# Kernel optimization log

Hardware: AMD Instinct MI355X
Metric: run time of the kernel (lower is better)

Reference implementation:

```python
import jax, jax.numpy as jnp
import numpy as np

C_IN = 128
C_INNER = 128


def setup_inputs() -> dict:
    key = jax.random.key(0)
    ks = jax.random.split(key, 9)
    b, c, h, w = 4, C_IN, 64, 64
    s = 1.0 / np.sqrt(c)
    x = jax.random.normal(ks[0], (b, c, h, w), dtype=jnp.float32)
    Wq = jax.random.normal(ks[1], (C_INNER, C_IN), dtype=jnp.float32) * s
    bq = jnp.zeros((C_INNER,), dtype=jnp.float32)
    Wk = jax.random.normal(ks[2], (C_INNER, C_IN), dtype=jnp.float32) * s
    bk = jnp.zeros((C_INNER,), dtype=jnp.float32)
    Wv = jax.random.normal(ks[3], (C_INNER, C_IN), dtype=jnp.float32) * s
    bv = jnp.zeros((C_INNER,), dtype=jnp.float32)
    Wo = jax.random.normal(ks[4], (C_IN, C_INNER), dtype=jnp.float32) * (1.0 / np.sqrt(C_INNER))
    bo = jnp.zeros((C_IN,), dtype=jnp.float32)
    return {"x": x, "Wq": Wq, "bq": bq, "Wk": Wk, "bk": bk,
            "Wv": Wv, "bv": bv, "Wo": Wo, "bo": bo}


def _conv1x1(x, W, bias):
    # x: (b,c,h,w), W: (o,c) -> (b,o,h,w)
    return jnp.einsum('oc,bchw->bohw', W, x) + bias[None, :, None, None]


def reference(x, Wq, bq, Wk, bk, Wv, bv, Wo, bo):
    b, c, h, w = x.shape
    ci = Wq.shape[0]
    n = h * w
    q = _conv1x1(x, Wq, bq).reshape(b, ci, n)          # (b, ci, n)
    k = _conv1x1(x, Wk, bk).reshape(b, ci, n)          # (b, ci, n)
    v = _conv1x1(x, Wv, bv).reshape(b, ci, n)          # (b, ci, n)
    # attn = softmax(q^T @ k) over keys
    attn = jnp.einsum('bci,bcj->bij', q, k)            # (b, n, n)
    attn = jax.nn.softmax(attn, axis=-1)
    out = jnp.einsum('bij,bcj->bci', attn, v)          # (b, ci, n)
    out = out.reshape(b, ci, h, w)
    out = _conv1x1(out, Wo, bo)
    return out + x
```

## Files before the change

kernel.cpp:

```cpp
#include <hip/hip_runtime.h>
#include <math.h>
#include <stdint.h>

#define CDIM 128
#define NTOT 4096

typedef _Float16 f16x8 __attribute__((ext_vector_type(8)));
typedef float floatx4 __attribute__((ext_vector_type(4)));

static __device__ __forceinline__ floatx4 mfma16(f16x8 a, f16x8 b, floatx4 c) {
    return __builtin_amdgcn_mfma_f32_16x16x32_f16(a, b, c, 0, 0, 0);
}
static __device__ __forceinline__ unsigned short f2h(float f) {
    _Float16 h = (_Float16)f;
    return __builtin_bit_cast(unsigned short, h);
}
static __device__ __forceinline__ float h2f(unsigned short u) {
    return (float)__builtin_bit_cast(_Float16, u);
}

#define SWZ(row, cc) ((((row) << 7)) + ((((cc) ^ ((row) & 15))) << 3))
#define SWZ8(row, cc) ((((row) << 6)) + ((((cc) ^ ((row) & 7))) << 3))

static __device__ __forceinline__ void gload_lds16(const void* g, void* l) {
    __builtin_amdgcn_global_load_lds(
        (const __attribute__((address_space(1))) void*)g,
        (__attribute__((address_space(3))) void*)l, 16, 0, 0);
}

__global__ __launch_bounds__(256) void wcvt_kernel(
    const float* __restrict__ Wq, const float* __restrict__ Wk,
    const float* __restrict__ Wv, const float* __restrict__ Wo,
    unsigned short* __restrict__ Wh)
{
    const float* src = (blockIdx.y == 0) ? Wq : (blockIdx.y == 1) ? Wk
                     : (blockIdx.y == 2) ? Wv : Wo;
    const int i = (blockIdx.x * 256 + threadIdx.x) * 4;
    float4 f = *(const float4*)&src[i];
    ushort4 u = { f2h(f.x), f2h(f.y), f2h(f.z), f2h(f.w) };
    *(ushort4*)&Wh[(size_t)blockIdx.y * 16384 + i] = u;
}

__global__ __launch_bounds__(256) void qkv_proj_kernel(
    const float* __restrict__ x, const unsigned short* __restrict__ Wh,
    const float* __restrict__ bq, const float* __restrict__ bk,
    const float* __restrict__ bv,
    unsigned short* __restrict__ qo, unsigned short* __restrict__ ko,
    unsigned short* __restrict__ vo)
{
    __shared__ __align__(16) unsigned short Xs[64][136];

    const int t = threadIdx.x, b = blockIdx.y, n0 = blockIdx.x * 64;
    const int zo = blockIdx.z * 64;
    const int w = t >> 6, quad = (t >> 4) & 3, l15 = t & 15;

    {
        const int n = (t & 15) * 4;
        const int c = (t >> 4) * 8;
        float4 xr[8];
        #pragma unroll
        for (int j = 0; j < 8; ++j)
            xr[j] = *(const float4*)&x[((size_t)b * CDIM + c + j) * NTOT + n0 + n];
        #pragma unroll
        for (int k = 0; k < 4; ++k) {
            ushort4 ulo, uhi;
            ulo.x = f2h(((const float*)&xr[0])[k]);
            ulo.y = f2h(((const float*)&xr[1])[k]);
            ulo.z = f2h(((const float*)&xr[2])[k]);
            ulo.w = f2h(((const float*)&xr[3])[k]);
            uhi.x = f2h(((const float*)&xr[4])[k]);
            uhi.y = f2h(((const float*)&xr[5])[k]);
            uhi.z = f2h(((const float*)&xr[6])[k]);
            uhi.w = f2h(((const float*)&xr[7])[k]);
            *(ushort4*)&Xs[n + k][c]     = ulo;
            *(ushort4*)&Xs[n + k][c + 4] = uhi;
        }
    }
    __syncthreads();

    f16x8 xf[4];
    #pragma unroll
    for (int f = 0; f < 4; ++f)
        xf[f] = *(const f16x8*)&Xs[w * 16 + l15][f * 32 + quad * 8];

    #pragma unroll
    for (int s = 0; s < 2; ++s) {
        const unsigned short* Wm = Wh + (size_t)s * 16384;
        const float* bias = s ? bk : bq;
        unsigned short* dst = s ? ko : qo;
        #pragma unroll
        for (int ot = 0; ot < 4; ++ot) {
            floatx4 acc = (floatx4){0.f, 0.f, 0.f, 0.f};
            #pragma unroll
            for (int f = 0; f < 4; ++f) {
                f16x8 aW = *(const f16x8*)
                    &Wm[(size_t)(zo + ot * 16 + l15) * CDIM + f * 32 + quad * 8];
                acc = mfma16(aW, xf[f], acc);
            }
            const int ob = zo + ot * 16 + quad * 4;
            ushort4 u;
            u.x = f2h(acc[0] + bias[ob + 0]);
            u.y = f2h(acc[1] + bias[ob + 1]);
            u.z = f2h(acc[2] + bias[ob + 2]);
            u.w = f2h(acc[3] + bias[ob + 3]);
            *(ushort4*)&dst[((size_t)b * NTOT + n0 + w * 16 + l15) * CDIM + ob] = u;
        }
    }
    {
        const unsigned short* Wm = Wh + 2 * 16384;
        #pragma unroll
        for (int ot = 0; ot < 4; ++ot) {
            floatx4 acc = (floatx4){0.f, 0.f, 0.f, 0.f};
            #pragma unroll
            for (int f = 0; f < 4; ++f) {
                f16x8 bW = *(const f16x8*)
                    &Wm[(size_t)(zo + ot * 16 + l15) * CDIM + f * 32 + quad * 8];
                acc = mfma16(xf[f], bW, acc);
            }
            const int o = zo + ot * 16 + l15;
            const float bv_ = bv[o];
            ushort4 u;
            u.x = f2h(acc[0] + bv_); u.y = f2h(acc[1] + bv_);
            u.z = f2h(acc[2] + bv_); u.w = f2h(acc[3] + bv_);
            *(ushort4*)&vo[((size_t)b * CDIM + o) * NTOT + n0 + w * 16 + quad * 4] = u;
        }
    }
}

__global__ __launch_bounds__(256, 3) void attn_kernel(
    const unsigned short* __restrict__ qg,
    const unsigned short* __restrict__ kg,
    const unsigned short* __restrict__ vg,
    unsigned short* __restrict__ Op,
    float* __restrict__ Ms, float* __restrict__ Ls)
{
    __shared__ __align__(16) unsigned short Kb[2][64 * 128];
    __shared__ __align__(16) unsigned short Vs[128 * 64];

    const int t = threadIdx.x;
    const int w = t >> 6, quad = (t >> 4) & 3, l15 = t & 15;

    const int bid = blockIdx.x;
    const int swz = ((bid & 7) << 6) | (bid >> 3);
    const int gidx = swz >> 5;
    const int b = gidx & 3;
    const int z = gidx >> 2;
    const int i0 = (swz & 31) * 128;
    const int jbase = z * 1024;
    const size_t vbase = (size_t)b * CDIM * NTOT;

    f16x8 bQ[2][4];
    #pragma unroll
    for (int nt = 0; nt < 2; ++nt) {
        const size_t qrow = ((size_t)b * NTOT + i0 + w * 32 + nt * 16 + l15) * CDIM;
        #pragma unroll
        for (int f = 0; f < 4; ++f)
            bQ[nt][f] = *(const f16x8*)&qg[qrow + f * 32 + quad * 8];
    }

    auto stageK = [&](unsigned short* Kd, int j0) {
        const size_t kbase = ((size_t)b * NTOT + j0) * CDIM;
        #pragma unroll
        for (int r = 0; r < 4; ++r) {
            const int flat = r * 256 + t;
            const int ldsoff = (r * 256 + (t & ~63)) * 8;
            const int krow = flat >> 4, kcc = flat & 15;
            gload_lds16(&kg[kbase + (size_t)krow * CDIM + ((kcc ^ (krow & 15)) << 3)],
                        &Kd[ldsoff]);
        }
    };
    auto stageV = [&](int j0) {
        const size_t vrow0 = vbase + j0;
        #pragma unroll
        for (int r = 0; r < 4; ++r) {
            const int flat = r * 256 + t;
            const int ldsoff = (r * 256 + (t & ~63)) * 8;
            const int vrow = flat >> 3, vcc = flat & 7;
            gload_lds16(&vg[vrow0 + (size_t)vrow * NTOT + ((vcc ^ (vrow & 7)) << 3)],
                        &Vs[ldsoff]);
        }
    };

    floatx4 accO[2][8];
    #pragma unroll
    for (int nt = 0; nt < 2; ++nt)
        #pragma unroll
        for (int dt = 0; dt < 8; ++dt) accO[nt][dt] = (floatx4){0.f, 0.f, 0.f, 0.f};
    float m_run[2] = {-INFINITY, -INFINITY};
    float l_part[2] = {0.f, 0.f};

    stageK(Kb[0], jbase);

    for (int iter = 0; iter < 16; ++iter) {
        const int cur = iter & 1;
        const int j0 = jbase + iter * 64;

        asm volatile("s_waitcnt vmcnt(0) lgkmcnt(0)" ::: "memory");
        __builtin_amdgcn_s_barrier();

        stageV(j0);
        if (iter < 15) stageK(Kb[cur ^ 1], j0 + 64);

        floatx4 accT[2][4];
        #pragma unroll
        for (int nt = 0; nt < 2; ++nt)
            #pragma unroll
            for (int jt = 0; jt < 4; ++jt) accT[nt][jt] = (floatx4){0.f, 0.f, 0.f, 0.f};
        #pragma unroll
        for (int jt = 0; jt < 4; ++jt)
            #pragma unroll
            for (int f = 0; f < 4; ++f) {
                f16x8 aK = *(const f16x8*)&Kb[cur][SWZ(jt * 16 + l15, f * 4 + quad)];
                accT[0][jt] = mfma16(aK, bQ[0][f], accT[0][jt]);
                accT[1][jt] = mfma16(aK, bQ[1][f], accT[1][jt]);
            }

        ushort4 pu[2][4];
        #pragma unroll
        for (int nt = 0; nt < 2; ++nt) {
            float tm = accT[nt][0][0];
            #pragma unroll
            for (int jt = 0; jt < 4; ++jt)
                #pragma unroll
                for (int r = 0; r < 4; ++r) tm = fmaxf(tm, accT[nt][jt][r]);
            tm = fmaxf(tm, __shfl_xor(tm, 16));
            tm = fmaxf(tm, __shfl_xor(tm, 32));
            if (__ballot(tm > m_run[nt] + 8.f)) {
                const float m_new = fmaxf(m_run[nt], tm);
                const float alpha = __expf(m_run[nt] - m_new);
                m_run[nt] = m_new;
                l_part[nt] *= alpha;
                #pragma unroll
                for (int dt = 0; dt < 8; ++dt) {
                    accO[nt][dt][0] *= alpha; accO[nt][dt][1] *= alpha;
                    accO[nt][dt][2] *= alpha; accO[nt][dt][3] *= alpha;
                }
            }
            const float mcur = m_run[nt];
            float ps = 0.f;
            #pragma unroll
            for (int jt = 0; jt < 4; ++jt) {
                float p0 = __expf(accT[nt][jt][0] - mcur);
                float p1 = __expf(accT[nt][jt][1] - mcur);
                float p2 = __expf(accT[nt][jt][2] - mcur);
                float p3 = __expf(accT[nt][jt][3] - mcur);
                ps += (p0 + p1) + (p2 + p3);
                pu[nt][jt].x = f2h(p0); pu[nt][jt].y = f2h(p1);
                pu[nt][jt].z = f2h(p2); pu[nt][jt].w = f2h(p3);
            }
            l_part[nt] += ps;
        }

        if (iter < 15)
            asm volatile("s_waitcnt lgkmcnt(0) vmcnt(4)" ::: "memory");
        else
            asm volatile("s_waitcnt lgkmcnt(0) vmcnt(0)" ::: "memory");
        __builtin_amdgcn_s_barrier();

        unsigned short* Pb = Kb[cur];
        #pragma unroll
        for (int nt = 0; nt < 2; ++nt) {
            const int prow = w * 32 + nt * 16 + l15;
            #pragma unroll
            for (int jt = 0; jt < 4; ++jt)
                *(ushort4*)&Pb[SWZ8(prow, 2 * jt + (quad >> 1)) + (quad & 1) * 4] =
                    pu[nt][jt];
        }

        f16x8 bP[2][2];
        #pragma unroll
        for (int nt = 0; nt < 2; ++nt) {
            const int prow = w * 32 + nt * 16 + l15;
            #pragma unroll
            for (int kb = 0; kb < 2; ++kb)
                bP[nt][kb] = *(const f16x8*)&Pb[SWZ8(prow, kb * 4 + quad)];
        }
        #pragma unroll
        for (int dt = 0; dt < 8; ++dt)
            #pragma unroll
            for (int kb = 0; kb < 2; ++kb) {
                f16x8 aV = *(const f16x8*)&Vs[SWZ8(dt * 16 + l15, kb * 4 + quad)];
                accO[0][dt] = mfma16(aV, bP[0][kb], accO[0][dt]);
                accO[1][dt] = mfma16(aV, bP[1][kb], accO[1][dt]);
            }
    }

    #pragma unroll
    for (int nt = 0; nt < 2; ++nt) {
        float lf = l_part[nt];
        lf += __shfl_xor(lf, 16);
        lf += __shfl_xor(lf, 32);
        const float inv = 1.0f / lf;
        const size_t orow =
            (((size_t)z * 4 + b) * NTOT + i0 + w * 32 + nt * 16 + l15) * CDIM;
        #pragma unroll
        for (int dt = 0; dt < 8; ++dt) {
            ushort4 u;
            u.x = f2h(accO[nt][dt][0] * inv); u.y = f2h(accO[nt][dt][1] * inv);
            u.z = f2h(accO[nt][dt][2] * inv); u.w = f2h(accO[nt][dt][3] * inv);
            *(ushort4*)&Op[orow + dt * 16 + quad * 4] = u;
        }
        if (quad == 0) {
            const int idx = (z * 4 + b) * NTOT + i0 + w * 32 + nt * 16 + l15;
            Ms[idx] = m_run[nt];
            Ls[idx] = lf;
        }
    }
}

__global__ __launch_bounds__(256) void out_proj_kernel(
    const unsigned short* __restrict__ Op,
    const float* __restrict__ Ms, const float* __restrict__ Ls,
    const unsigned short* __restrict__ Woh, const float* __restrict__ bo,
    const float* __restrict__ x, float* __restrict__ out)
{
    __shared__ __align__(16) unsigned short As[64][136];

    const int t = threadIdx.x, b = blockIdx.y, n0 = blockIdx.x * 64;
    const int zo = blockIdx.z * 64;
    const int w = t >> 6, quad = (t >> 4) & 3, l15 = t & 15;

    const size_t PER = (size_t)NTOT * 4 * CDIM;

    #pragma unroll
    for (int r = 0; r < 4; ++r) {
        int flat = r * 256 + t;
        int row = flat >> 4, c16 = (flat & 15) * 8;
        const int bn = b * NTOT + n0 + row;
        float m0 = Ms[bn], m1 = Ms[bn + 16384], m2 = Ms[bn + 32768], m3 = Ms[bn + 49152];
        float M = fmaxf(fmaxf(m0, m1), fmaxf(m2, m3));
        float w0 = Ls[bn]         * __expf(m0 - M);
        float w1 = Ls[bn + 16384] * __expf(m1 - M);
        float w2 = Ls[bn + 32768] * __expf(m2 - M);
        float w3 = Ls[bn + 49152] * __expf(m3 - M);
        const float inv = 1.0f / (w0 + w1 + w2 + w3);
        w0 *= inv; w1 *= inv; w2 *= inv; w3 *= inv;

        const size_t base = (size_t)bn * CDIM + c16;
        uint4 a0 = *(const uint4*)&Op[base];
        uint4 a1 = *(const uint4*)&Op[PER + base];
        uint4 a2 = *(const uint4*)&Op[2 * PER + base];
        uint4 a3 = *(const uint4*)&Op[3 * PER + base];
        const unsigned short* p0 = (const unsigned short*)&a0;
        const unsigned short* p1 = (const unsigned short*)&a1;
        const unsigned short* p2 = (const unsigned short*)&a2;
        const unsigned short* p3 = (const unsigned short*)&a3;
        unsigned short mv[8];
        #pragma unroll
        for (int j = 0; j < 8; ++j)
            mv[j] = f2h(w0 * h2f(p0[j]) + w1 * h2f(p1[j]) +
                        w2 * h2f(p2[j]) + w3 * h2f(p3[j]));
        *(uint4*)&As[row][c16] = *(const uint4*)mv;
    }
    __syncthreads();

    f16x8 bA[4];
    #pragma unroll
    for (int f = 0; f < 4; ++f)
        bA[f] = *(const f16x8*)&As[w * 16 + l15][f * 32 + quad * 8];

    #pragma unroll
    for (int ot = 0; ot < 4; ++ot) {
        floatx4 acc = (floatx4){0.f, 0.f, 0.f, 0.f};
        #pragma unroll
        for (int f = 0; f < 4; ++f) {
            f16x8 aW = *(const f16x8*)
                &Woh[(size_t)(zo + ot * 16 + l15) * CDIM + f * 32 + quad * 8];
            acc = mfma16(aW, bA[f], acc);
        }
        const int ob = zo + ot * 16 + quad * 4;
        #pragma unroll
        for (int r = 0; r < 4; ++r) {
            size_t idx = ((size_t)b * CDIM + ob + r) * NTOT + n0 + w * 16 + l15;
            out[idx] = acc[r] + bo[ob + r] + x[idx];
        }
    }
}

extern "C" void kernel_launch(void* const* d_in, const int* in_sizes, int n_in,
                              void* d_out, int out_size, void* d_ws, size_t ws_size,
                              hipStream_t stream)
{
    const float* x  = (const float*)d_in[0];
    const float* Wq = (const float*)d_in[1];
    const float* bq = (const float*)d_in[2];
    const float* Wk = (const float*)d_in[3];
    const float* bk = (const float*)d_in[4];
    const float* Wv = (const float*)d_in[5];
    const float* bv = (const float*)d_in[6];
    const float* Wo = (const float*)d_in[7];
    const float* bo = (const float*)d_in[8];
    float* out = (float*)d_out;

    const size_t PER = (size_t)4 * CDIM * NTOT;
    unsigned short* q_ws  = (unsigned short*)d_ws;
    unsigned short* k_ws  = q_ws + PER;
    unsigned short* v_ws  = k_ws + PER;
    unsigned short* op_ws = v_ws + PER;
    float*          ms_ws = (float*)(op_ws + 4 * PER);
    float*          ls_ws = ms_ws + 4 * 16384;
    unsigned short* wh_ws = (unsigned short*)(ls_ws + 4 * 16384);

    wcvt_kernel<<<dim3(16, 4), dim3(256), 0, stream>>>(Wq, Wk, Wv, Wo, wh_ws);
    qkv_proj_kernel<<<dim3(64, 4, 2), dim3(256), 0, stream>>>(
        x, wh_ws, bq, bk, bv, q_ws, k_ws, v_ws);
    attn_kernel<<<dim3(512, 1, 1), dim3(256), 0, stream>>>(
        q_ws, k_ws, v_ws, op_ws, ms_ws, ls_ws);
    out_proj_kernel<<<dim3(64, 4, 2), dim3(256), 0, stream>>>(
        op_ws, ms_ws, ls_ws, wh_ws + 3 * 16384, bo, x, out);
}
```

Before: 161.4 us.

## Double-buffer V tiles in attention, add dedicated P buffer, retile projection kernels

Result: faster. 150.5 us (-6.7%).

```diff
diff --git a/kernel.cpp b/kernel.cpp
--- a/kernel.cpp
+++ b/kernel.cpp
@@ -48,32 +48,28 @@
     unsigned short* __restrict__ qo, unsigned short* __restrict__ ko,
     unsigned short* __restrict__ vo)
 {
-    __shared__ __align__(16) unsigned short Xs[64][136];
-
-    const int t = threadIdx.x, b = blockIdx.y, n0 = blockIdx.x * 64;
-    const int zo = blockIdx.z * 64;
+    __shared__ __align__(16) unsigned short Xs[16][136];
+
+    const int t = threadIdx.x;
+    const int bid = blockIdx.x;
+    const int swz = ((bid & 7) << 7) | (bid >> 3);
+    const int b = swz >> 8;
+    const int n0 = (swz & 255) * 16;
     const int w = t >> 6, quad = (t >> 4) & 3, l15 = t & 15;
 
     {
-        const int n = (t & 15) * 4;
-        const int c = (t >> 4) * 8;
-        float4 xr[8];
-        #pragma unroll
-        for (int j = 0; j < 8; ++j)
+        const int n = (t & 3) * 4;
+        const int c = (t >> 2) * 2;
+        float4 xr[2];
+        #pragma unroll
+        for (int j = 0; j < 2; ++j)
             xr[j] = *(const float4*)&x[((size_t)b * CDIM + c + j) * NTOT + n0 + n];
         #pragma unroll
         for (int k = 0; k < 4; ++k) {
-            ushort4 ulo, uhi;
-            ulo.x = f2h(((const float*)&xr[0])[k]);
-            ulo.y = f2h(((const float*)&xr[1])[k]);
-            ulo.z = f2h(((const float*)&xr[2])[k]);
-            ulo.w = f2h(((const float*)&xr[3])[k]);
-            uhi.x = f2h(((const float*)&xr[4])[k]);
-            uhi.y = f2h(((const float*)&xr[5])[k]);
-            uhi.z = f2h(((const float*)&xr[6])[k]);
-            uhi.w = f2h(((const float*)&xr[7])[k]);
-            *(ushort4*)&Xs[n + k][c]     = ulo;
-            *(ushort4*)&Xs[n + k][c + 4] = uhi;
+            ushort2 u;
+            u.x = f2h(((const float*)&xr[0])[k]);
+            u.y = f2h(((const float*)&xr[1])[k]);
+            *(ushort2*)&Xs[n + k][c] = u;
         }
     }
     __syncthreads();
@@ -81,7 +77,7 @@
     f16x8 xf[4];
     #pragma unroll
     for (int f = 0; f < 4; ++f)
-        xf[f] = *(const f16x8*)&Xs[w * 16 + l15][f * 32 + quad * 8];
+        xf[f] = *(const f16x8*)&Xs[l15][f * 32 + quad * 8];
 
     #pragma unroll
     for (int s = 0; s < 2; ++s) {
@@ -89,45 +85,46 @@
         const float* bias = s ? bk : bq;
         unsigned short* dst = s ? ko : qo;
         #pragma unroll
-        for (int ot = 0; ot < 4; ++ot) {
+        for (int ot = 0; ot < 2; ++ot) {
+            const int o = w * 32 + ot * 16;
             floatx4 acc = (floatx4){0.f, 0.f, 0.f, 0.f};
             #pragma unroll
             for (int f = 0; f < 4; ++f) {
                 f16x8 aW = *(const f16x8*)
-                    &Wm[(size_t)(zo + ot * 16 + l15) * CDIM + f * 32 + quad * 8];
+                    &Wm[(size_t)(o + l15) * CDIM + f * 32 + quad * 8];
                 acc = mfma16(aW, xf[f], acc);
             }
-            const int ob = zo + ot * 16 + quad * 4;
+            const int ob = o + quad * 4;
             ushort4 u;
             u.x = f2h(acc[0] + bias[ob + 0]);
             u.y = f2h(acc[1] + bias[ob + 1]);
             u.z = f2h(acc[2] + bias[ob + 2]);
             u.w = f2h(acc[3] + bias[ob + 3]);
-            *(ushort4*)&dst[((size_t)b * NTOT + n0 + w * 16 + l15) * CDIM + ob] = u;
+            *(ushort4*)&dst[((size_t)b * NTOT + n0 + l15) * CDIM + ob] = u;
         }
     }
     {
         const unsigned short* Wm = Wh + 2 * 16384;
         #pragma unroll
-        for (int ot = 0; ot < 4; ++ot) {
+        for (int ot = 0; ot < 2; ++ot) {
+            const int o = w * 32 + ot * 16 + l15;
             floatx4 acc = (floatx4){0.f, 0.f, 0.f, 0.f};
             #pragma unroll
             for (int f = 0; f < 4; ++f) {
                 f16x8 bW = *(const f16x8*)
-                    &Wm[(size_t)(zo + ot * 16 + l15) * CDIM + f * 32 + quad * 8];
+                    &Wm[(size_t)o * CDIM + f * 32 + quad * 8];
                 acc = mfma16(xf[f], bW, acc);
             }
-            const int o = zo + ot * 16 + l15;
             const float bv_ = bv[o];
             ushort4 u;
             u.x = f2h(acc[0] + bv_); u.y = f2h(acc[1] + bv_);
             u.z = f2h(acc[2] + bv_); u.w = f2h(acc[3] + bv_);
-            *(ushort4*)&vo[((size_t)b * CDIM + o) * NTOT + n0 + w * 16 + quad * 4] = u;
-        }
-    }
-}
-
-__global__ __launch_bounds__(256, 3) void attn_kernel(
+            *(ushort4*)&vo[((size_t)b * CDIM + o) * NTOT + n0 + quad * 4] = u;
+        }
+    }
+}
+
+__global__ __launch_bounds__(256, 2) void attn_kernel(
     const unsigned short* __restrict__ qg,
     const unsigned short* __restrict__ kg,
     const unsigned short* __restrict__ vg,
@@ -135,7 +132,8 @@
     float* __restrict__ Ms, float* __restrict__ Ls)
 {
     __shared__ __align__(16) unsigned short Kb[2][64 * 128];
-    __shared__ __align__(16) unsigned short Vs[128 * 64];
+    __shared__ __align__(16) unsigned short Vb[2][128 * 64];
+    __shared__ __align__(16) unsigned short Ps[128 * 64];
 
     const int t = threadIdx.x;
     const int w = t >> 6, quad = (t >> 4) & 3, l15 = t & 15;
@@ -158,8 +156,9 @@
             bQ[nt][f] = *(const f16x8*)&qg[qrow + f * 32 + quad * 8];
     }
 
-    auto stageK = [&](unsigned short* Kd, int j0) {
+    auto stage = [&](unsigned short* Kd, unsigned short* Vd, int j0) {
         const size_t kbase = ((size_t)b * NTOT + j0) * CDIM;
+        const size_t vrow0 = vbase + j0;
         #pragma unroll
         for (int r = 0; r < 4; ++r) {
             const int flat = r * 256 + t;
@@ -168,16 +167,13 @@
             gload_lds16(&kg[kbase + (size_t)krow * CDIM + ((kcc ^ (krow & 15)) << 3)],
                         &Kd[ldsoff]);
         }
-    };
-    auto stageV = [&](int j0) {
-        const size_t vrow0 = vbase + j0;
         #pragma unroll
         for (int r = 0; r < 4; ++r) {
             const int flat = r * 256 + t;
             const int ldsoff = (r * 256 + (t & ~63)) * 8;
             const int vrow = flat >> 3, vcc = flat & 7;
             gload_lds16(&vg[vrow0 + (size_t)vrow * NTOT + ((vcc ^ (vrow & 7)) << 3)],
-                        &Vs[ldsoff]);
+                        &Vd[ldsoff]);
         }
     };
 
@@ -189,23 +185,22 @@
     float m_run[2] = {-INFINITY, -INFINITY};
     float l_part[2] = {0.f, 0.f};
 
-    stageK(Kb[0], jbase);
+    stage(Kb[0], Vb[0], jbase);
 
     for (int iter = 0; iter < 16; ++iter) {
         const int cur = iter & 1;
-        const int j0 = jbase + iter * 64;
 
         asm volatile("s_waitcnt vmcnt(0) lgkmcnt(0)" ::: "memory");
         __builtin_amdgcn_s_barrier();
 
-        stageV(j0);
-        if (iter < 15) stageK(Kb[cur ^ 1], j0 + 64);
+        if (iter < 15) stage(Kb[cur ^ 1], Vb[cur ^ 1], jbase + (iter + 1) * 64);
 
         floatx4 accT[2][4];
         #pragma unroll
         for (int nt = 0; nt < 2; ++nt)
             #pragma unroll
             for (int jt = 0; jt < 4; ++jt) accT[nt][jt] = (floatx4){0.f, 0.f, 0.f, 0.f};
+        __builtin_amdgcn_s_setprio(1);
         #pragma unroll
         for (int jt = 0; jt < 4; ++jt)
             #pragma unroll
@@ -214,6 +209,7 @@
                 accT[0][jt] = mfma16(aK, bQ[0][f], accT[0][jt]);
                 accT[1][jt] = mfma16(aK, bQ[1][f], accT[1][jt]);
             }
+        __builtin_amdgcn_s_setprio(0);
 
         ushort4 pu[2][4];
         #pragma unroll
@@ -251,21 +247,16 @@
             l_part[nt] += ps;
         }
 
-        if (iter < 15)
-            asm volatile("s_waitcnt lgkmcnt(0) vmcnt(4)" ::: "memory");
-        else
-            asm volatile("s_waitcnt lgkmcnt(0) vmcnt(0)" ::: "memory");
-        __builtin_amdgcn_s_barrier();
-
-        unsigned short* Pb = Kb[cur];
         #pragma unroll
         for (int nt = 0; nt < 2; ++nt) {
             const int prow = w * 32 + nt * 16 + l15;
             #pragma unroll
             for (int jt = 0; jt < 4; ++jt)
-                *(ushort4*)&Pb[SWZ8(prow, 2 * jt + (quad >> 1)) + (quad & 1) * 4] =
+                *(ushort4*)&Ps[SWZ8(prow, 2 * jt + (quad >> 1)) + (quad & 1) * 4] =
                     pu[nt][jt];
         }
+        asm volatile("s_waitcnt lgkmcnt(0)" ::: "memory");
+        __builtin_amdgcn_sched_barrier(0);
 
         f16x8 bP[2][2];
         #pragma unroll
@@ -273,16 +264,18 @@
             const int prow = w * 32 + nt * 16 + l15;
             #pragma unroll
             for (int kb = 0; kb < 2; ++kb)
-                bP[nt][kb] = *(const f16x8*)&Pb[SWZ8(prow, kb * 4 + quad)];
-        }
+                bP[nt][kb] = *(const f16x8*)&Ps[SWZ8(prow, kb * 4 + quad)];
+        }
+        __builtin_amdgcn_s_setprio(1);
         #pragma unroll
         for (int dt = 0; dt < 8; ++dt)
             #pragma unroll
             for (int kb = 0; kb < 2; ++kb) {
-                f16x8 aV = *(const f16x8*)&Vs[SWZ8(dt * 16 + l15, kb * 4 + quad)];
+                f16x8 aV = *(const f16x8*)&Vb[cur][SWZ8(dt * 16 + l15, kb * 4 + quad)];
                 accO[0][dt] = mfma16(aV, bP[0][kb], accO[0][dt]);
                 accO[1][dt] = mfma16(aV, bP[1][kb], accO[1][dt]);
             }
+        __builtin_amdgcn_s_setprio(0);
     }
 
     #pragma unroll
@@ -314,16 +307,16 @@
     const unsigned short* __restrict__ Woh, const float* __restrict__ bo,
     const float* __restrict__ x, float* __restrict__ out)
 {
-    __shared__ __align__(16) unsigned short As[64][136];
-
-    const int t = threadIdx.x, b = blockIdx.y, n0 = blockIdx.x * 64;
+    __shared__ __align__(16) unsigned short As[32][136];
+
+    const int t = threadIdx.x, b = blockIdx.y, n0 = blockIdx.x * 32;
     const int zo = blockIdx.z * 64;
     const int w = t >> 6, quad = (t >> 4) & 3, l15 = t & 15;
 
     const size_t PER = (size_t)NTOT * 4 * CDIM;
 
     #pragma unroll
-    for (int r = 0; r < 4; ++r) {
+    for (int r = 0; r < 2; ++r) {
         int flat = r * 256 + t;
         int row = flat >> 4, c16 = (flat & 15) * 8;
         const int bn = b * NTOT + n0 + row;
@@ -354,24 +347,26 @@
     }
     __syncthreads();
 
+    const int nt = w & 1, oh = w >> 1;
     f16x8 bA[4];
     #pragma unroll
     for (int f = 0; f < 4; ++f)
-        bA[f] = *(const f16x8*)&As[w * 16 + l15][f * 32 + quad * 8];
-
-    #pragma unroll
-    for (int ot = 0; ot < 4; ++ot) {
+        bA[f] = *(const f16x8*)&As[nt * 16 + l15][f * 32 + quad * 8];
+
+    #pragma unroll
+    for (int ot = 0; ot < 2; ++ot) {
+        const int o = zo + oh * 32 + ot * 16;
         floatx4 acc = (floatx4){0.f, 0.f, 0.f, 0.f};
         #pragma unroll
         for (int f = 0; f < 4; ++f) {
             f16x8 aW = *(const f16x8*)
-                &Woh[(size_t)(zo + ot * 16 + l15) * CDIM + f * 32 + quad * 8];
+                &Woh[(size_t)(o + l15) * CDIM + f * 32 + quad * 8];
             acc = mfma16(aW, bA[f], acc);
         }
-        const int ob = zo + ot * 16 + quad * 4;
+        const int ob = o + quad * 4;
         #pragma unroll
         for (int r = 0; r < 4; ++r) {
-            size_t idx = ((size_t)b * CDIM + ob + r) * NTOT + n0 + w * 16 + l15;
+            size_t idx = ((size_t)b * CDIM + ob + r) * NTOT + n0 + nt * 16 + l15;
             out[idx] = acc[r] + bo[ob + r] + x[idx];
         }
     }
@@ -402,10 +397,10 @@
     unsigned short* wh_ws = (unsigned short*)(ls_ws + 4 * 16384);
 
     wcvt_kernel<<<dim3(16, 4), dim3(256), 0, stream>>>(Wq, Wk, Wv, Wo, wh_ws);
-    qkv_proj_kernel<<<dim3(64, 4, 2), dim3(256), 0, stream>>>(
+    qkv_proj_kernel<<<dim3(1024), dim3(256), 0, stream>>>(
         x, wh_ws, bq, bk, bv, q_ws, k_ws, v_ws);
-    attn_kernel<<<dim3(512, 1, 1), dim3(256), 0, stream>>>(
+    attn_kernel<<<dim3(512), dim3(256), 0, stream>>>(
         q_ws, k_ws, v_ws, op_ws, ms_ws, ls_ws);
-    out_proj_kernel<<<dim3(64, 4, 2), dim3(256), 0, stream>>>(
+    out_proj_kernel<<<dim3(128, 4, 2), dim3(256), 0, stream>>>(
         op_ws, ms_ws, ls_ws, wh_ws + 3 * 16384, bo, x, out);
 }
```
